# Optimization experiments

Hardware: AMD Instinct MI355X
Metric: run time of the kernel (lower is better)

Reference implementation:

```python
import jax, jax.numpy as jnp
import numpy as np
from jax import lax

B, EMB, CIN, COUT, K, H, W = 16, 768, 64, 64, 3, 112, 112
HID = EMB // 4  # reduction_ratio=4
TOTAL = COUT * CIN * K * K


def setup_inputs() -> dict:
    key = jax.random.key(0)
    k1, k2, k3, k4 = jax.random.split(key, 4)
    cls_token = jax.random.normal(k1, (B, 1, EMB), dtype=jnp.float32)
    features = jax.random.normal(k2, (B, CIN, H, W), dtype=jnp.float32)
    W1 = jax.random.normal(k3, (EMB, HID), dtype=jnp.float32) * 0.02
    b1 = jnp.zeros((HID,), dtype=jnp.float32)
    W2 = jax.random.normal(k4, (HID, TOTAL), dtype=jnp.float32) * 0.01
    b2 = jnp.zeros((TOTAL,), dtype=jnp.float32)
    return {"cls_token": cls_token, "features": features,
            "W1": W1, "b1": b1, "W2": W2, "b2": b2}


def _per_sample_conv(feat, kern):
    # feat: (CIN, H, W); kern: (COUT, CIN, K, K) -> (COUT, H, W)
    out = lax.conv_general_dilated(
        feat[None], kern, window_strides=(1, 1), padding="SAME",
        dimension_numbers=("NCHW", "OIHW", "NCHW"))
    return out[0]


def reference(cls_token, features, W1, b1, W2, b2):
    # Dynamic kernel generation from CLS token
    x = cls_token[:, 0, :]                      # (B, EMB)
    h = jax.nn.relu(x @ W1 + b1)                # (B, HID)
    params = jnp.tanh(h @ W2 + b2)              # (B, TOTAL)
    kernel = params.reshape(B, COUT, CIN, K, K)
    # Per-sample convolution (equivalent to unfold + bmm in torch)
    conv_feat = jax.vmap(_per_sample_conv)(features, kernel)  # (B, COUT, H, W)
    # in_channels == out_channels -> identity shortcut
    return conv_feat + features
```

## Files before the change

### kernel.cpp

```cpp
#include <hip/hip_runtime.h>
#include <hip/hip_bf16.h>

#define BB   16
#define EMB  768
#define CIN  64
#define COUT 64
#define HH   112
#define WW   112
#define HID  192
#define TOTAL 36864
#define KSZ  576
#define PW   114
#define CELL 128
#define ROWB (PW * CELL)

typedef short bf16x8 __attribute__((ext_vector_type(8)));
typedef float f32x4  __attribute__((ext_vector_type(4)));
typedef int   i32x4  __attribute__((ext_vector_type(4)));

static __device__ __forceinline__ unsigned short f2bf(float f) {
    unsigned u = __float_as_uint(f);
    u += 0x7FFF + ((u >> 16) & 1);
    return (unsigned short)(u >> 16);
}

static __device__ __forceinline__ bf16x8 pack8(const float* v) {
    bf16x8 r;
    #pragma unroll
    for (int j = 0; j < 8; ++j) r[j] = (short)f2bf(v[j]);
    return r;
}

#define GLOAD_LDS16(g, l) \
    __builtin_amdgcn_global_load_lds((const __attribute__((address_space(1))) void*)(g), \
                                     (__attribute__((address_space(3))) void*)(l), 16, 0, 0)

__global__ __launch_bounds__(256) void pre_mlp1(const float* __restrict__ feat,
                                                unsigned short* __restrict__ P,
                                                const float* __restrict__ cls,
                                                const float* __restrict__ W1,
                                                const float* __restrict__ b1,
                                                float* __restrict__ h) {
    __shared__ float smem[EMB + 16 * 17];
    const int bid = blockIdx.x;
    const int tid = threadIdx.x;

    if (bid < HH * BB) {
        const int b = bid & 15;
        const int y = bid >> 4;
        unsigned short* Prow = P + ((size_t)b * PW + y + 1) * (PW * 64);
        if (tid < 16) {
            const int cell = (tid >> 3) ? (PW - 1) : 0;
            *(i32x4*)((char*)Prow + cell * CELL + (tid & 7) * 16) = (i32x4){0, 0, 0, 0};
        }
        const int o = tid >> 5;
        const int q = tid & 31;
        if (q < 28) {
            const float* fb = feat + (((size_t)b * CIN + o * 8) * HH + y) * WW + 4 * q;
            f32x4 v[8];
            #pragma unroll
            for (int j = 0; j < 8; ++j) v[j] = *(const f32x4*)(fb + (size_t)j * (HH * WW));
            #pragma unroll
            for (int i = 0; i < 4; ++i) {
                unsigned short w[8];
                #pragma unroll
                for (int j = 0; j < 8; ++j) w[j] = f2bf(v[j][i]);
                *(bf16x8*)(Prow + (size_t)(4 * q + i + 1) * 64 + o * 8) = *(bf16x8*)w;
            }
        }
    } else if (bid < HH * BB + 32) {
        const int idx = bid - HH * BB;
        const int b = idx & 15;
        unsigned short* Prow = P + ((size_t)b * PW + ((idx >> 4) ? (PW - 1) : 0)) * (PW * 64);
        #pragma unroll
        for (int k = 0; k < 4; ++k) {
            const int i = tid + 256 * k;
            if (i < 912) ((i32x4*)Prow)[i] = (i32x4){0, 0, 0, 0};
        }
    } else {
        float* xs  = smem;
        float* red = smem + EMB;
        const int idx = bid - (HH * BB + 32);
        const int b   = idx / 12;
        const int jg  = idx - 12 * b;
        for (int i = tid; i < EMB; i += 256) xs[i] = cls[b * EMB + i];
        __syncthreads();
        const int j16 = tid & 15;
        const int kq  = tid >> 4;
        const int j   = jg * 16 + j16;
        float acc = 0.f;
        #pragma unroll
        for (int k = kq * 48; k < kq * 48 + 48; ++k) acc += xs[k] * W1[k * HID + j];
        red[j16 * 17 + kq] = acc;
        __syncthreads();
        if (tid < 16) {
            float s = b1[jg * 16 + tid];
            #pragma unroll
            for (int q = 0; q < 16; ++q) s += red[tid * 17 + q];
            h[b * HID + jg * 16 + tid] = fmaxf(s, 0.f);
        }
    }
}

__global__ __launch_bounds__(256) void mlp2_kernel(const float* __restrict__ h,
                                                   const float* __restrict__ W2,
                                                   const float* __restrict__ b2,
                                                   unsigned short* __restrict__ Ag) {
    __shared__ float hs[16 * 193];
    const int tid = threadIdx.x;
    for (int i = tid; i < BB * HID; i += 256) {
        const int bb = i / HID;
        hs[bb * 193 + (i - bb * HID)] = h[i];
    }
    __syncthreads();
    const int wave = tid >> 6;
    const int lane = tid & 63;
    const int lg   = lane >> 4;
    const int ln   = lane & 15;
    const int t0   = (blockIdx.x * 4 + wave) * 16;

    bf16x8 a6[6];
    #pragma unroll
    for (int kk = 0; kk < 6; ++kk) {
        float v[8];
        #pragma unroll
        for (int j = 0; j < 8; ++j) v[j] = hs[ln * 193 + kk * 32 + lg * 8 + j];
        a6[kk] = pack8(v);
    }

    f32x4 acc = (f32x4){0.f, 0.f, 0.f, 0.f};
    #pragma unroll
    for (int kk = 0; kk < 6; ++kk) {
        float w[8];
        #pragma unroll
        for (int j = 0; j < 8; ++j)
            w[j] = W2[(size_t)(kk * 32 + lg * 8 + j) * TOTAL + t0 + ln];
        acc = __builtin_amdgcn_mfma_f32_16x16x32_bf16(a6[kk], pack8(w), acc, 0, 0, 0);
    }

    const int t    = t0 + ln;
    const float bias = b2[t];
    const int co  = t / KSZ;
    const int rem = t - co * KSZ;
    const int ci  = rem / 9;
    const int p9  = rem - ci * 9;
    const float idv = (p9 == 4 && co == ci) ? 1.f : 0.f;
    unsigned short* pA = Ag + (size_t)(p9 * 64 + co) * 64 + ci;
    #pragma unroll
    for (int rg = 0; rg < 4; ++rg) {
        const int bi = lg * 4 + rg;
        pA[(size_t)bi * TOTAL] = f2bf(tanhf(acc[rg] + bias) + idv);
    }
}

__global__ __launch_bounds__(256) void conv_kernel(const unsigned short* __restrict__ Ag,
                                                   const unsigned short* __restrict__ P,
                                                   float* __restrict__ out) {
    __shared__ __align__(16) char lds[4 * ROWB];
    const int tid = threadIdx.x;
    const int bid  = (blockIdx.x & 7) * 112 + (blockIdx.x >> 3);
    const int b    = bid / 56;
    const int tile = bid - b * 56;
    const int y0   = tile * 2;

    const char* Prow0 = (const char*)(P + ((size_t)b * PW + y0) * (PW * 64));
    #pragma unroll
    for (int it = 0; it < 14; ++it) {
        const int i = it * 256 + tid;
        const int s = i / 912;
        const int j = i - s * 912;
        const int c = j >> 3, g = j & 7;
        GLOAD_LDS16(Prow0 + (size_t)s * ROWB + c * CELL + ((g ^ (c & 7)) << 4),
                    lds + (size_t)i * 16);
    }
    if (tid < 64) {
        const int i = 3584 + tid;
        const int j = i - 3 * 912;
        const int c = j >> 3, g = j & 7;
        GLOAD_LDS16(Prow0 + (size_t)3 * ROWB + c * CELL + ((g ^ (c & 7)) << 4),
                    lds + (size_t)i * 16);
    }

    const int wave = tid >> 6;
    const int lane = tid & 63;
    const int cog  = wave & 1;
    const int r    = wave >> 1;
    const int lg   = lane >> 4;
    const int ln   = lane & 15;
    const unsigned short* Ab = Ag + (size_t)b * 9 * 4096;
    bf16x8 af[9][2][2];
    #pragma unroll
    for (int p9 = 0; p9 < 9; ++p9)
        #pragma unroll
        for (int ct = 0; ct < 2; ++ct)
            #pragma unroll
            for (int cib = 0; cib < 2; ++cib)
                af[p9][ct][cib] = *(const bf16x8*)(Ab + (size_t)(p9 * 64 + cog * 32 + ct * 16 + ln) * 64
                                                   + cib * 32 + lg * 8);
    __syncthreads();

    f32x4 acc[2][7];
    #pragma unroll
    for (int ct = 0; ct < 2; ++ct)
        #pragma unroll
        for (int t = 0; t < 7; ++t) acc[ct][t] = (f32x4){0.f, 0.f, 0.f, 0.f};

    #pragma unroll
    for (int p9 = 0; p9 < 9; ++p9) {
        const int kh = p9 / 3, kw = p9 - 3 * kh;
        const char* lbase = lds + (r + kh) * ROWB + (ln + kw) * CELL;
        const int   c7    = (ln + kw) & 7;
        #pragma unroll
        for (int cib = 0; cib < 2; ++cib) {
            const int sw = ((cib * 4 + lg) ^ c7) << 4;
            #pragma unroll
            for (int t = 0; t < 7; ++t) {
                const bf16x8 bf = *(const bf16x8*)(lbase + t * 2048 + sw);
                acc[0][t] = __builtin_amdgcn_mfma_f32_16x16x32_bf16(af[p9][0][cib], bf, acc[0][t], 0, 0, 0);
                acc[1][t] = __builtin_amdgcn_mfma_f32_16x16x32_bf16(af[p9][1][cib], bf, acc[1][t], 0, 0, 0);
            }
        }
    }

    const int y = y0 + r;
    float* ob = out + (((size_t)b * COUT + cog * 32 + lg * 4) * HH + y) * WW + ln;
    #pragma unroll
    for (int ct = 0; ct < 2; ++ct)
        #pragma unroll
        for (int t = 0; t < 7; ++t)
            #pragma unroll
            for (int rg = 0; rg < 4; ++rg)
                ob[((size_t)(ct * 16 + rg)) * HH * WW + t * 16] = acc[ct][t][rg];
}

extern "C" void kernel_launch(void* const* d_in, const int* in_sizes, int n_in,
                              void* d_out, int out_size, void* d_ws, size_t ws_size,
                              hipStream_t stream) {
    const float* cls      = (const float*)d_in[0];
    const float* features = (const float*)d_in[1];
    const float* W1       = (const float*)d_in[2];
    const float* b1       = (const float*)d_in[3];
    const float* W2       = (const float*)d_in[4];
    const float* b2       = (const float*)d_in[5];
    float* out = (float*)d_out;

    float*          h  = (float*)d_ws;
    unsigned short* Ag = (unsigned short*)(h + BB * HID);
    unsigned short* P  = Ag + (size_t)BB * 9 * 4096;

    pre_mlp1<<<HH * BB + 32 + 192, 256, 0, stream>>>(features, P, cls, W1, b1, h);
    mlp2_kernel<<<TOTAL / 64, 256, 0, stream>>>(h, W2, b2, Ag);
    conv_kernel<<<56 * BB, 256, 0, stream>>>(Ag, P, out);
}
```

Measured before the change: 60.58 us.

## Process 8-row strips per block with 6-row LDS ring and prefetch

The conv kernel now has each block compute an 8-row output strip instead of 2 rows, launching 224 persistent-style blocks. Input rows stream through a 6-row LDS ring buffer, with the next two rows prefetched via global_load_lds while the current rows are computed. vmcnt waits sized to exclude the output stores keep the prefetch overlapped with compute. This cuts halo re-reads and per-block weight fragment loads, but lowers occupancy to one block per CU and leaves some CUs idle.

```diff
diff --git a/kernel.cpp b/kernel.cpp
--- a/kernel.cpp
+++ b/kernel.cpp
@@ -13,6 +13,7 @@
 #define PW   114
 #define CELL 128
 #define ROWB (PW * CELL)
+#define RING 6
 
 typedef short bf16x8 __attribute__((ext_vector_type(8)));
 typedef float f32x4  __attribute__((ext_vector_type(4)));
@@ -34,6 +35,9 @@
 #define GLOAD_LDS16(g, l) \
     __builtin_amdgcn_global_load_lds((const __attribute__((address_space(1))) void*)(g), \
                                      (__attribute__((address_space(3))) void*)(l), 16, 0, 0)
+
+#define WAIT_VMCNT(n) do { asm volatile("s_waitcnt vmcnt(" #n ")" ::: "memory"); \
+                           __builtin_amdgcn_sched_barrier(0); } while (0)
 
 __global__ __launch_bounds__(256) void pre_mlp1(const float* __restrict__ feat,
                                                 unsigned short* __restrict__ P,
@@ -153,33 +157,15 @@
     }
 }
 
-__global__ __launch_bounds__(256) void conv_kernel(const unsigned short* __restrict__ Ag,
-                                                   const unsigned short* __restrict__ P,
-                                                   float* __restrict__ out) {
-    __shared__ __align__(16) char lds[4 * ROWB];
+__global__ __launch_bounds__(256, 1) void conv_kernel(const unsigned short* __restrict__ Ag,
+                                                      const unsigned short* __restrict__ P,
+                                                      float* __restrict__ out) {
+    extern __shared__ __align__(16) char lds[];
     const int tid = threadIdx.x;
-    const int bid  = (blockIdx.x & 7) * 112 + (blockIdx.x >> 3);
-    const int b    = bid / 56;
-    const int tile = bid - b * 56;
-    const int y0   = tile * 2;
-
-    const char* Prow0 = (const char*)(P + ((size_t)b * PW + y0) * (PW * 64));
-    #pragma unroll
-    for (int it = 0; it < 14; ++it) {
-        const int i = it * 256 + tid;
-        const int s = i / 912;
-        const int j = i - s * 912;
-        const int c = j >> 3, g = j & 7;
-        GLOAD_LDS16(Prow0 + (size_t)s * ROWB + c * CELL + ((g ^ (c & 7)) << 4),
-                    lds + (size_t)i * 16);
-    }
-    if (tid < 64) {
-        const int i = 3584 + tid;
-        const int j = i - 3 * 912;
-        const int c = j >> 3, g = j & 7;
-        GLOAD_LDS16(Prow0 + (size_t)3 * ROWB + c * CELL + ((g ^ (c & 7)) << 4),
-                    lds + (size_t)i * 16);
-    }
+    const int bid   = (blockIdx.x & 7) * 28 + (blockIdx.x >> 3);
+    const int b     = bid / 14;
+    const int strip = bid - b * 14;
+    const int Y0    = strip * 8;
 
     const int wave = tid >> 6;
     const int lane = tid & 63;
@@ -187,6 +173,7 @@
     const int r    = wave >> 1;
     const int lg   = lane >> 4;
     const int ln   = lane & 15;
+
     const unsigned short* Ab = Ag + (size_t)b * 9 * 4096;
     bf16x8 af[9][2][2];
     #pragma unroll
@@ -197,40 +184,88 @@
             for (int cib = 0; cib < 2; ++cib)
                 af[p9][ct][cib] = *(const bf16x8*)(Ab + (size_t)(p9 * 64 + cog * 32 + ct * 16 + ln) * 64
                                                    + cib * 32 + lg * 8);
-    __syncthreads();
-
-    f32x4 acc[2][7];
-    #pragma unroll
-    for (int ct = 0; ct < 2; ++ct)
-        #pragma unroll
-        for (int t = 0; t < 7; ++t) acc[ct][t] = (f32x4){0.f, 0.f, 0.f, 0.f};
-
-    #pragma unroll
-    for (int p9 = 0; p9 < 9; ++p9) {
-        const int kh = p9 / 3, kw = p9 - 3 * kh;
-        const char* lbase = lds + (r + kh) * ROWB + (ln + kw) * CELL;
-        const int   c7    = (ln + kw) & 7;
-        #pragma unroll
-        for (int cib = 0; cib < 2; ++cib) {
-            const int sw = ((cib * 4 + lg) ^ c7) << 4;
-            #pragma unroll
-            for (int t = 0; t < 7; ++t) {
-                const bf16x8 bf = *(const bf16x8*)(lbase + t * 2048 + sw);
-                acc[0][t] = __builtin_amdgcn_mfma_f32_16x16x32_bf16(af[p9][0][cib], bf, acc[0][t], 0, 0, 0);
-                acc[1][t] = __builtin_amdgcn_mfma_f32_16x16x32_bf16(af[p9][1][cib], bf, acc[1][t], 0, 0, 0);
+
+    const char* Pb = (const char*)P + ((size_t)b * PW + Y0) * ROWB;
+
+    if (tid < 228) {
+        #pragma unroll
+        for (int k = 0; k < 16; ++k) {
+            const int i = k * 228 + tid;
+            const int s = i / 912, jj = i - s * 912;
+            const int c = jj >> 3, g = jj & 7;
+            GLOAD_LDS16(Pb + (size_t)s * ROWB + c * CELL + ((g ^ (c & 7)) << 4),
+                        lds + (size_t)i * 16);
+        }
+    }
+    WAIT_VMCNT(0);
+    __builtin_amdgcn_s_barrier();
+    __builtin_amdgcn_sched_barrier(0);
+
+    #pragma unroll
+    for (int t = 0; t < 4; ++t) {
+        if (t > 0) {
+            WAIT_VMCNT(56);
+            __builtin_amdgcn_s_barrier();
+            __builtin_amdgcn_sched_barrier(0);
+        }
+        if (t < 3) {
+            const int lr0 = 2 * t + 4;
+            const int s0  = lr0 % RING;
+            const char* Ps = Pb + (size_t)lr0 * ROWB;
+            char* ldst = lds + (size_t)s0 * ROWB;
+            if (tid < 228) {
+                #pragma unroll
+                for (int k = 0; k < 8; ++k) {
+                    const int i = k * 228 + tid;
+                    const int s = i / 912, jj = i - s * 912;
+                    const int c = jj >> 3, g = jj & 7;
+                    GLOAD_LDS16(Ps + (size_t)s * ROWB + c * CELL + ((g ^ (c & 7)) << 4),
+                                ldst + (size_t)i * 16);
+                }
             }
         }
-    }
-
-    const int y = y0 + r;
-    float* ob = out + (((size_t)b * COUT + cog * 32 + lg * 4) * HH + y) * WW + ln;
-    #pragma unroll
-    for (int ct = 0; ct < 2; ++ct)
-        #pragma unroll
-        for (int t = 0; t < 7; ++t)
-            #pragma unroll
-            for (int rg = 0; rg < 4; ++rg)
-                ob[((size_t)(ct * 16 + rg)) * HH * WW + t * 16] = acc[ct][t][rg];
+
+        const char* rp[3];
+        #pragma unroll
+        for (int kh = 0; kh < 3; ++kh) {
+            const int lr = 2 * t + r + kh;
+            const int sl = lr - (lr >= RING ? RING : 0);
+            rp[kh] = lds + (size_t)sl * ROWB;
+        }
+
+        f32x4 acc[2][7];
+        #pragma unroll
+        for (int ct = 0; ct < 2; ++ct)
+            #pragma unroll
+            for (int tt = 0; tt < 7; ++tt) acc[ct][tt] = (f32x4){0.f, 0.f, 0.f, 0.f};
+
+        #pragma unroll
+        for (int p9 = 0; p9 < 9; ++p9) {
+            const int kh = p9 / 3, kw = p9 - 3 * kh;
+            const char* lbase = rp[kh] + (ln + kw) * CELL;
+            const int   c7    = (ln + kw) & 7;
+            #pragma unroll
+            for (int cib = 0; cib < 2; ++cib) {
+                const int sw = ((cib * 4 + lg) ^ c7) << 4;
+                #pragma unroll
+                for (int tt = 0; tt < 7; ++tt) {
+                    const bf16x8 bf = *(const bf16x8*)(lbase + tt * (16 * CELL) + sw);
+                    acc[0][tt] = __builtin_amdgcn_mfma_f32_16x16x32_bf16(af[p9][0][cib], bf, acc[0][tt], 0, 0, 0);
+                    acc[1][tt] = __builtin_amdgcn_mfma_f32_16x16x32_bf16(af[p9][1][cib], bf, acc[1][tt], 0, 0, 0);
+                }
+            }
+        }
+
+        const int y = Y0 + 2 * t + r;
+        float* ob = out + (((size_t)b * COUT + cog * 32 + lg * 4) * HH + y) * WW + ln;
+        #pragma unroll
+        for (int ct = 0; ct < 2; ++ct)
+            #pragma unroll
+            for (int tt = 0; tt < 7; ++tt)
+                #pragma unroll
+                for (int rg = 0; rg < 4; ++rg)
+                    ob[((size_t)(ct * 16 + rg)) * HH * WW + tt * 16] = acc[ct][tt][rg];
+    }
 }
 
 extern "C" void kernel_launch(void* const* d_in, const int* in_sizes, int n_in,
@@ -248,7 +283,10 @@
     unsigned short* Ag = (unsigned short*)(h + BB * HID);
     unsigned short* P  = Ag + (size_t)BB * 9 * 4096;
 
+    (void)hipFuncSetAttribute((const void*)conv_kernel,
+                              hipFuncAttributeMaxDynamicSharedMemorySize, RING * ROWB);
+
     pre_mlp1<<<HH * BB + 32 + 192, 256, 0, stream>>>(features, P, cls, W1, b1, h);
     mlp2_kernel<<<TOTAL / 64, 256, 0, stream>>>(h, W2, b2, Ag);
-    conv_kernel<<<56 * BB, 256, 0, stream>>>(Ag, P, out);
-}
+    conv_kernel<<<224, 256, RING * ROWB, stream>>>(Ag, P, out);
+}
```

New measurement: 59.76 us. Within noise of the previous version (-1.4%).

## Restructure conv tiles to 4-row strips with channel-halved LDS staging

Applied to the files above, without the earlier changes.

Each conv block now computes a 4-row strip across all 64 output channels, one row per wave, instead of a 2-row tile split into channel groups. It stages the padded input in two halves of 32 input channels into a smaller LDS buffer, with a new swizzle. Weight fragments are loaded per tap rather than all held in registers up front. This aims to cut redundant halo loads and register pressure so three blocks fit per CU. In exchange it adds a barrier between the two halves and issues more global weight loads inside the MMA loop.

```diff
diff --git a/kernel.cpp b/kernel.cpp
--- a/kernel.cpp
+++ b/kernel.cpp
@@ -13,6 +13,9 @@
 #define PW   114
 #define CELL 128
 #define ROWB (PW * CELL)
+#define CELLH 64
+#define LROW (PW * CELLH)
+#define NCHUNK (6 * PW * 4)
 
 typedef short bf16x8 __attribute__((ext_vector_type(8)));
 typedef float f32x4  __attribute__((ext_vector_type(4)));
@@ -153,79 +156,75 @@
     }
 }
 
-__global__ __launch_bounds__(256) void conv_kernel(const unsigned short* __restrict__ Ag,
-                                                   const unsigned short* __restrict__ P,
-                                                   float* __restrict__ out) {
-    __shared__ __align__(16) char lds[4 * ROWB];
+__global__ __launch_bounds__(256, 3) void conv_kernel(const unsigned short* __restrict__ Ag,
+                                                      const unsigned short* __restrict__ P,
+                                                      float* __restrict__ out) {
+    __shared__ __align__(16) char lds[6 * LROW];
     const int tid = threadIdx.x;
-    const int bid  = (blockIdx.x & 7) * 112 + (blockIdx.x >> 3);
-    const int b    = bid / 56;
-    const int tile = bid - b * 56;
-    const int y0   = tile * 2;
-
-    const char* Prow0 = (const char*)(P + ((size_t)b * PW + y0) * (PW * 64));
-    #pragma unroll
-    for (int it = 0; it < 14; ++it) {
-        const int i = it * 256 + tid;
-        const int s = i / 912;
-        const int j = i - s * 912;
-        const int c = j >> 3, g = j & 7;
-        GLOAD_LDS16(Prow0 + (size_t)s * ROWB + c * CELL + ((g ^ (c & 7)) << 4),
-                    lds + (size_t)i * 16);
-    }
-    if (tid < 64) {
-        const int i = 3584 + tid;
-        const int j = i - 3 * 912;
-        const int c = j >> 3, g = j & 7;
-        GLOAD_LDS16(Prow0 + (size_t)3 * ROWB + c * CELL + ((g ^ (c & 7)) << 4),
-                    lds + (size_t)i * 16);
-    }
+    const int bid   = (blockIdx.x & 7) * 56 + (blockIdx.x >> 3);
+    const int b     = bid / 28;
+    const int strip = bid - b * 28;
+    const int y0    = strip * 4;
 
     const int wave = tid >> 6;
     const int lane = tid & 63;
-    const int cog  = wave & 1;
-    const int r    = wave >> 1;
     const int lg   = lane >> 4;
     const int ln   = lane & 15;
+
     const unsigned short* Ab = Ag + (size_t)b * 9 * 4096;
-    bf16x8 af[9][2][2];
-    #pragma unroll
-    for (int p9 = 0; p9 < 9; ++p9)
-        #pragma unroll
-        for (int ct = 0; ct < 2; ++ct)
-            #pragma unroll
-            for (int cib = 0; cib < 2; ++cib)
-                af[p9][ct][cib] = *(const bf16x8*)(Ab + (size_t)(p9 * 64 + cog * 32 + ct * 16 + ln) * 64
-                                                   + cib * 32 + lg * 8);
-    __syncthreads();
-
-    f32x4 acc[2][7];
-    #pragma unroll
-    for (int ct = 0; ct < 2; ++ct)
+    const char* Pb = (const char*)P + ((size_t)b * PW + y0) * ROWB;
+
+    f32x4 acc[4][7];
+    #pragma unroll
+    for (int ct = 0; ct < 4; ++ct)
         #pragma unroll
         for (int t = 0; t < 7; ++t) acc[ct][t] = (f32x4){0.f, 0.f, 0.f, 0.f};
 
     #pragma unroll
-    for (int p9 = 0; p9 < 9; ++p9) {
-        const int kh = p9 / 3, kw = p9 - 3 * kh;
-        const char* lbase = lds + (r + kh) * ROWB + (ln + kw) * CELL;
-        const int   c7    = (ln + kw) & 7;
-        #pragma unroll
-        for (int cib = 0; cib < 2; ++cib) {
-            const int sw = ((cib * 4 + lg) ^ c7) << 4;
+    for (int h = 0; h < 2; ++h) {
+        if (h) __syncthreads();
+        #pragma unroll
+        for (int k = 0; k < 11; ++k) {
+            const int i = k * 256 + tid;
+            if (i < NCHUNK) {
+                const int s    = i / (PW * 4);
+                const int rem  = i - s * (PW * 4);
+                const int cell = rem >> 2;
+                const int sl   = rem & 3;
+                const int g    = sl ^ (cell & 3);
+                GLOAD_LDS16(Pb + (size_t)s * ROWB + cell * CELL + h * 64 + g * 16,
+                            lds + (size_t)i * 16);
+            }
+        }
+        asm volatile("s_waitcnt vmcnt(0)" ::: "memory");
+        __builtin_amdgcn_s_barrier();
+        __builtin_amdgcn_sched_barrier(0);
+
+        #pragma unroll
+        for (int p9 = 0; p9 < 9; ++p9) {
+            const int kh = p9 / 3, kw = p9 - 3 * kh;
+            bf16x8 af[4];
+            #pragma unroll
+            for (int ct = 0; ct < 4; ++ct)
+                af[ct] = *(const bf16x8*)(Ab + (size_t)(p9 * 64 + ct * 16 + ln) * 64
+                                          + h * 32 + lg * 8);
+            const char* lbase = lds + (wave + kh) * LROW;
             #pragma unroll
             for (int t = 0; t < 7; ++t) {
-                const bf16x8 bf = *(const bf16x8*)(lbase + t * 2048 + sw);
-                acc[0][t] = __builtin_amdgcn_mfma_f32_16x16x32_bf16(af[p9][0][cib], bf, acc[0][t], 0, 0, 0);
-                acc[1][t] = __builtin_amdgcn_mfma_f32_16x16x32_bf16(af[p9][1][cib], bf, acc[1][t], 0, 0, 0);
+                const int cell = ln + kw + 16 * t;
+                const int sl   = lg ^ (cell & 3);
+                const bf16x8 bf = *(const bf16x8*)(lbase + cell * CELLH + sl * 16);
+                #pragma unroll
+                for (int ct = 0; ct < 4; ++ct)
+                    acc[ct][t] = __builtin_amdgcn_mfma_f32_16x16x32_bf16(af[ct], bf, acc[ct][t], 0, 0, 0);
             }
         }
     }
 
-    const int y = y0 + r;
-    float* ob = out + (((size_t)b * COUT + cog * 32 + lg * 4) * HH + y) * WW + ln;
-    #pragma unroll
-    for (int ct = 0; ct < 2; ++ct)
+    const int y = y0 + wave;
+    float* ob = out + (((size_t)b * COUT + lg * 4) * HH + y) * WW + ln;
+    #pragma unroll
+    for (int ct = 0; ct < 4; ++ct)
         #pragma unroll
         for (int t = 0; t < 7; ++t)
             #pragma unroll
@@ -250,5 +249,5 @@
 
     pre_mlp1<<<HH * BB + 32 + 192, 256, 0, stream>>>(features, P, cls, W1, b1, h);
     mlp2_kernel<<<TOTAL / 64, 256, 0, stream>>>(h, W2, b2, Ag);
-    conv_kernel<<<56 * BB, 256, 0, stream>>>(Ag, P, out);
-}
+    conv_kernel<<<448, 256, 0, stream>>>(Ag, P, out);
+}
```

After: 86.10 us. 1.42x slower.
